# Optimization experiments

Hardware: AMD Instinct MI355X
Metric: run time of the kernel (lower is better)

## Reference

```python
import jax, jax.numpy as jnp
import numpy as np

TOPK = 10
NC = 80
ALPHA = 1.0
BETA = 6.0
EPS = 1e-8
IOU_EPS = 1e-7


def setup_inputs() -> dict:
    key = jax.random.key(0)
    ks = jax.random.split(key, 7)
    B, M, C = 32, 40, NC
    img = 640
    pts = []
    for s in (8, 16, 32):
        n = img // s
        xs = (jnp.arange(n, dtype=jnp.float32) + 0.5) * s
        gy, gx = jnp.meshgrid(xs, xs, indexing="ij")
        pts.append(jnp.stack([gx.ravel(), gy.ravel()], axis=-1))
    anchor_points = jnp.concatenate(pts, axis=0)  # (8400, 2)
    A = anchor_points.shape[0]
    pred_scores = jax.random.uniform(ks[0], (B, A, C), dtype=jnp.float32)
    ctr = anchor_points[None] + jax.random.normal(ks[1], (B, A, 2), dtype=jnp.float32) * 8.0
    wh = jax.random.uniform(ks[2], (B, A, 2), minval=16.0, maxval=128.0, dtype=jnp.float32)
    pred_boxes = jnp.concatenate([ctr - wh / 2, ctr + wh / 2], axis=-1)
    gctr = jax.random.uniform(ks[3], (B, M, 2), minval=64.0, maxval=576.0, dtype=jnp.float32)
    gwh = jax.random.uniform(ks[4], (B, M, 2), minval=32.0, maxval=256.0, dtype=jnp.float32)
    gt_boxes = jnp.concatenate([gctr - gwh / 2, gctr + gwh / 2], axis=-1)
    gt_labels = jax.random.randint(ks[5], (B, M, 1), 0, C)
    gt_mask = jax.random.uniform(ks[6], (B, M, 1)) < 0.8
    return {
        "pred_scores": pred_scores,
        "pred_boxes": pred_boxes,
        "anchor_points": anchor_points,
        "gt_labels": gt_labels,
        "gt_boxes": gt_boxes,
        "gt_mask": gt_mask,
    }


def reference(pred_scores, pred_boxes, anchor_points, gt_labels, gt_boxes, gt_mask):
    B, A, C = pred_scores.shape
    M = gt_boxes.shape[1]
    dt = pred_scores.dtype
    gtm = gt_mask[..., 0].astype(dt)  # (B, M)
    cls = gt_labels[..., 0].astype(jnp.int32)  # (B, M)
    b_idx = jnp.arange(B)[:, None]

    # --- step 1: anchor centers inside GT boxes ---
    lt = gt_boxes[:, :, None, :2]  # (B, M, 1, 2)
    rb = gt_boxes[:, :, None, 2:]
    ap = anchor_points[None, None, :, :]  # (1, 1, A, 2)
    deltas = jnp.concatenate([ap - lt, rb - ap], axis=-1)  # (B, M, A, 4)
    in_gt = (jnp.min(deltas, axis=-1) > EPS).astype(dt)  # (B, M, A)
    valid = in_gt * gtm[:, :, None]

    # --- alignment metric: cls score gathered per GT label, IoU(gt, pred) ---
    scores = pred_scores[b_idx, :, cls] * valid  # (B, M, A)
    gt = gt_boxes[:, :, None, :]  # (B, M, 1, 4)
    pd = pred_boxes[:, None, :, :]  # (B, 1, A, 4)
    iw = jnp.clip(jnp.minimum(gt[..., 2], pd[..., 2]) - jnp.maximum(gt[..., 0], pd[..., 0]), 0.0)
    ih = jnp.clip(jnp.minimum(gt[..., 3], pd[..., 3]) - jnp.maximum(gt[..., 1], pd[..., 1]), 0.0)
    inter = iw * ih
    area_g = (gt[..., 2] - gt[..., 0]) * (gt[..., 3] - gt[..., 1])
    area_p = (pd[..., 2] - pd[..., 0]) * (pd[..., 3] - pd[..., 1])
    ious = jnp.clip(inter / (area_g + area_p - inter + IOU_EPS), 0.0) * valid  # (B, M, A)
    align = (scores ** ALPHA) * (ious ** BETA)

    # --- step 2: top-k candidates per GT with duplicate suppression ---
    _, topk_idxs = jax.lax.top_k(align, TOPK)  # (B, M, K)
    km = jnp.broadcast_to(gt_mask[..., 0][:, :, None], topk_idxs.shape)
    topk_idxs = jnp.where(km, topk_idxs, 0)
    counts = jnp.zeros((B, M, A), dtype=jnp.int32)
    counts = counts.at[b_idx[:, :, None], jnp.arange(M)[None, :, None], topk_idxs].add(1)
    counts = jnp.where(counts > 1, 0, counts)
    mask = counts.astype(dt) * in_gt * gtm[:, :, None]  # (B, M, A)

    # --- step 4: resolve anchors assigned to multiple GTs by highest IoU ---
    fg = mask.sum(axis=1)  # (B, A)
    max_iou_onehot = jax.nn.one_hot(jnp.argmax(ious, axis=1), M, axis=1, dtype=dt)
    mask = jnp.where(fg[:, None, :] > 1, max_iou_onehot, mask)
    fg = mask.sum(axis=1)
    tgt_idx = jnp.argmax(mask, axis=1)  # (B, A)

    # --- targets ---
    target_labels = jnp.clip(jnp.take_along_axis(cls, tgt_idx, axis=1), 0, NC)  # (B, A)
    target_boxes = jnp.take_along_axis(gt_boxes, tgt_idx[..., None], axis=1)  # (B, A, 4)
    target_scores = jax.nn.one_hot(target_labels, NC, dtype=dt)
    target_scores = jnp.where(fg[..., None] > 0, target_scores, 0.0)

    # --- normalize scores by aligned metric ---
    align = align * mask
    pos_align = jnp.max(align, axis=-1, keepdims=True)  # (B, M, 1)
    pos_iou = jnp.max(ious * mask, axis=-1, keepdims=True)
    norm = jnp.max(align * pos_iou / (pos_align + EPS), axis=-2)[..., None]  # (B, A, 1)
    target_scores = target_scores * norm
    return target_labels, target_boxes, target_scores, fg > 0
```

## Files before the change

### kernel.cpp

```cpp
#include <hip/hip_runtime.h>
#include <cstdint>

#define TOPK_K 10
#define NCLS   80
#define EPS_F     1e-8f
#define IOU_EPS_F 1e-7f

typedef unsigned long long u64;

#define INS10(val, idx)                                                     \
    {                                                                       \
        u64 key = ((u64)__float_as_uint(val) << 32) |                       \
                  (unsigned)(~(unsigned)(idx));                             \
        if (key > kk[9]) {                                                  \
            _Pragma("unroll")                                               \
            for (int q = 0; q < 10; ++q) {                                  \
                if (key > kk[q]) { u64 t_ = kk[q]; kk[q] = key; key = t_; } \
            }                                                               \
        }                                                                   \
    }

__global__ void k_init(const unsigned char* __restrict__ gm, int n,
                       int* __restrict__ gmask,
                       unsigned int* __restrict__ pos_a,
                       unsigned int* __restrict__ pos_i,
                       u64* __restrict__ mask_bits, int BA)
{
    const int stride = gridDim.x * blockDim.x;
    for (int i = blockIdx.x * blockDim.x + threadIdx.x; i < BA; i += stride)
        mask_bits[i] = 0ull;

    if (blockIdx.x == 0) {
        __shared__ int anynz;
        if (threadIdx.x == 0) anynz = 0;
        __syncthreads();
        for (int i = threadIdx.x; i < n; i += blockDim.x) {
            if ((i & 3) && gm[i]) anynz = 1;
        }
        __syncthreads();
        const int is_int32 = (anynz == 0);
        const int* gi = (const int*)gm;
        for (int i = threadIdx.x; i < n; i += blockDim.x) {
            gmask[i] = is_int32 ? (gi[i] != 0) : (gm[i] != 0);
            pos_a[i] = 0u;
            pos_i[i] = 0u;
        }
    }
}

__global__ __launch_bounds__(256) void k_topk_geo(
    const float*  __restrict__ ps,
    const float4* __restrict__ pb,
    const int*    __restrict__ gl,
    const float4* __restrict__ gb,
    const int*    __restrict__ gmask,
    u64*          __restrict__ mask_bits,
    int B, int A, int C, int M)
{
    const int bm = blockIdx.x;
    if (!gmask[bm]) return;
    const int b = bm / M;
    const int m = bm - b * M;
    const int tid = threadIdx.x;

    const float4 g = gb[bm];
    const float areag = (g.z - g.x) * (g.w - g.y);
    const int cls = gl[bm];
    const float*  psb = ps + (size_t)b * A * C + cls;
    const float4* pbb = pb + (size_t)b * A;

    u64 kk[10];
#pragma unroll
    for (int q = 0; q < 10; ++q) kk[q] = 0ull;

    if (tid < 64) {
        const float x = (tid + 0.5f) * 8.0f;
        const float y = 4.0f;
        const float d = fminf(fminf(x - g.x, y - g.y),
                              fminf(g.z - x, g.w - y));
        const u64 inb  = __ballot(d > EPS_F);
        const u64 outb = ~inb;
        if (((outb >> tid) & 1ull) &&
            __popcll(outb & ((1ull << tid) - 1ull)) < TOPK_K) {
            INS10(0.0f, tid);
        }
    }

#define LEVEL(SS, NN, BASE)                                                   \
    {                                                                         \
        const float s_ = (float)(SS); const int n_ = (NN);                    \
        const int jlo = max(0,      (int)floorf(g.x / s_ - 0.5f));            \
        const int jhi = min(n_ - 1, (int)ceilf (g.z / s_ - 0.5f));            \
        const int ilo = max(0,      (int)floorf(g.y / s_ - 0.5f));            \
        const int ihi = min(n_ - 1, (int)ceilf (g.w / s_ - 0.5f));            \
        const int nx = jhi - jlo + 1, ny = ihi - ilo + 1;                     \
        const int tot = (nx > 0 && ny > 0) ? nx * ny : 0;                     \
        for (int c = tid; c < tot; c += 256) {                                \
            const int ci = c / nx, cj = c - ci * nx;                          \
            const int i = ilo + ci, j = jlo + cj;                             \
            const float x = (j + 0.5f) * s_, y = (i + 0.5f) * s_;             \
            const float d = fminf(fminf(x - g.x, y - g.y),                    \
                                  fminf(g.z - x, g.w - y));                   \
            if (d > EPS_F) {                                                  \
                const int a = (BASE) + i * n_ + j;                            \
                const float4 p = pbb[a];                                      \
                const float iw = fmaxf(fminf(g.z, p.z) - fmaxf(g.x, p.x), 0.f);\
                const float ih = fmaxf(fminf(g.w, p.w) - fmaxf(g.y, p.y), 0.f);\
                const float inter = iw * ih;                                  \
                const float areap = (p.z - p.x) * (p.w - p.y);                \
                const float iou = fmaxf(inter / (areag + areap - inter + IOU_EPS_F), 0.f); \
                const float sc = psb[(size_t)a * C];                          \
                const float i2 = iou * iou;                                   \
                const float al = sc * (i2 * i2 * i2);                         \
                INS10(al, a);                                                 \
            }                                                                 \
        }                                                                     \
    }
    LEVEL(8,  80, 0)
    LEVEL(16, 40, 6400)
    LEVEL(32, 20, 8000)
#undef LEVEL

    __shared__ u64 swv[4];
    const u64 bit = 1ull << m;
    for (int r = 0; r < TOPK_K; ++r) {
        u64 cur = kk[0];
#pragma unroll
        for (int off = 32; off; off >>= 1) {
            const u64 o = __shfl_xor(cur, off);
            cur = (o > cur) ? o : cur;
        }
        if ((tid & 63) == 0) swv[tid >> 6] = cur;
        __syncthreads();
        const u64 w01 = (swv[0] > swv[1]) ? swv[0] : swv[1];
        const u64 w23 = (swv[2] > swv[3]) ? swv[2] : swv[3];
        const u64 win = (w01 > w23) ? w01 : w23;
        if (kk[0] == win) {
#pragma unroll
            for (int q = 0; q < 9; ++q) kk[q] = kk[q + 1];
            kk[9] = 0ull;
        }
        if (tid == 0 && win != 0ull) {
            const unsigned a = ~(unsigned)(win & 0xFFFFFFFFull);
            float x, y;
            if (a < 6400u) {
                const unsigned i = a / 80u, j = a - i * 80u;
                x = (j + 0.5f) * 8.0f;  y = (i + 0.5f) * 8.0f;
            } else if (a < 8000u) {
                const unsigned rr = a - 6400u;
                const unsigned i = rr / 40u, j = rr - i * 40u;
                x = (j + 0.5f) * 16.0f; y = (i + 0.5f) * 16.0f;
            } else {
                const unsigned rr = a - 8000u;
                const unsigned i = rr / 20u, j = rr - i * 20u;
                x = (j + 0.5f) * 32.0f; y = (i + 0.5f) * 32.0f;
            }
            const float d = fminf(fminf(x - g.x, y - g.y),
                                  fminf(g.z - x, g.w - y));
            if (d > EPS_F)
                atomicOr(&mask_bits[(size_t)b * A + a], bit);
        }
        __syncthreads();
    }
}

__global__ __launch_bounds__(256) void k_topk_fb(
    const float*  __restrict__ ps, const float4* __restrict__ pb,
    const float2* __restrict__ apts, const int* __restrict__ gl,
    const float4* __restrict__ gb, const int* __restrict__ gmask,
    u64* __restrict__ mask_bits, int B, int A, int C, int M)
{
    const int bm = blockIdx.x;
    if (!gmask[bm]) return;
    const int b = bm / M;
    const int m = bm - b * M;
    const float4 g = gb[bm];
    const float areag = (g.z - g.x) * (g.w - g.y);
    const int cls = gl[bm];
    const float*  psb = ps + (size_t)b * A * C + cls;
    const float4* pbb = pb + (size_t)b * A;
    const int tid = threadIdx.x;

    u64 kk[10];
#pragma unroll
    for (int q = 0; q < 10; ++q) kk[q] = 0ull;

    for (int a = tid; a < A; a += 256) {
        const float2 an = apts[a];
        const float d = fminf(fminf(an.x - g.x, an.y - g.y),
                              fminf(g.z - an.x, g.w - an.y));
        float al = 0.0f;
        if (d > EPS_F) {
            const float4 p = pbb[a];
            const float iw = fmaxf(fminf(g.z, p.z) - fmaxf(g.x, p.x), 0.0f);
            const float ih = fmaxf(fminf(g.w, p.w) - fmaxf(g.y, p.y), 0.0f);
            const float inter = iw * ih;
            const float areap = (p.z - p.x) * (p.w - p.y);
            const float iou = fmaxf(inter / (areag + areap - inter + IOU_EPS_F), 0.0f);
            const float sc = psb[(size_t)a * C];
            const float i2 = iou * iou;
            al = sc * (i2 * i2 * i2);
        }
        INS10(al, a);
    }

    __shared__ u64 swv[4];
    const u64 bit = 1ull << m;
    for (int r = 0; r < TOPK_K; ++r) {
        u64 cur = kk[0];
#pragma unroll
        for (int off = 32; off; off >>= 1) {
            const u64 o = __shfl_xor(cur, off);
            cur = (o > cur) ? o : cur;
        }
        if ((tid & 63) == 0) swv[tid >> 6] = cur;
        __syncthreads();
        const u64 w01 = (swv[0] > swv[1]) ? swv[0] : swv[1];
        const u64 w23 = (swv[2] > swv[3]) ? swv[2] : swv[3];
        const u64 win = (w01 > w23) ? w01 : w23;
        if (kk[0] == win) {
#pragma unroll
            for (int q = 0; q < 9; ++q) kk[q] = kk[q + 1];
            kk[9] = 0ull;
        }
        if (tid == 0 && win != 0ull) {
            const unsigned a = ~(unsigned)(win & 0xFFFFFFFFull);
            const float2 an = apts[a];
            const float d = fminf(fminf(an.x - g.x, an.y - g.y),
                                  fminf(g.z - an.x, g.w - an.y));
            if (d > EPS_F)
                atomicOr(&mask_bits[(size_t)b * A + a], bit);
        }
        __syncthreads();
    }
}

__global__ __launch_bounds__(256) void k_resolve(
    const float*  __restrict__ ps,
    const float4* __restrict__ pb,
    const float2* __restrict__ apts,
    const int*    __restrict__ gl,
    const float4* __restrict__ gb,
    const int*    __restrict__ gmask,
    const u64*    __restrict__ mask_bits,
    int*          __restrict__ assign,
    float*        __restrict__ aval,
    unsigned int* __restrict__ pos_align,
    unsigned int* __restrict__ pos_iou,
    float*        __restrict__ out,
    int B, int A, int C, int M)
{
    const int id = blockIdx.x * blockDim.x + threadIdx.x;
    if (id >= B * A) return;
    const int b = id / A;
    const int a = id - b * A;

    const u64 bits = mask_bits[id];

    if (bits == 0ull) {
        assign[id] = 0;
        aval[id]   = 0.0f;
        int lab = gl[b * M];
        lab = lab < 0 ? 0 : (lab > NCLS ? NCLS : lab);
        out[id] = (float)lab;
        ((float4*)(out + (size_t)B * A))[id] = gb[b * M];
        out[(size_t)B * A * (5 + NCLS) + id] = 0.0f;
        return;
    }

    const int cnt = __popcll(bits);
    int t;
    const float2 an = apts[a];
    const float4 p  = pb[id];
    const float areap = (p.z - p.x) * (p.w - p.y);

    if (cnt == 1) {
        t = __ffsll(bits) - 1;
    } else {
        float best = -1.0f; int bi = 0;
        for (int mm = 0; mm < M; ++mm) {
            const float4 gg = gb[b * M + mm];
            const float d = fminf(fminf(an.x - gg.x, an.y - gg.y),
                                  fminf(gg.z - an.x, gg.w - an.y));
            float iou = 0.0f;
            if (d > EPS_F && gmask[b * M + mm]) {
                const float iw = fmaxf(fminf(gg.z, p.z) - fmaxf(gg.x, p.x), 0.0f);
                const float ih = fmaxf(fminf(gg.w, p.w) - fmaxf(gg.y, p.y), 0.0f);
                const float inter = iw * ih;
                const float areag = (gg.z - gg.x) * (gg.w - gg.y);
                iou = fmaxf(inter / (areag + areap - inter + IOU_EPS_F), 0.0f);
            }
            if (iou > best) { best = iou; bi = mm; }
        }
        t = bi;
    }

    float av = 0.0f;
    {
        const float4 gg = gb[b * M + t];
        const float d = fminf(fminf(an.x - gg.x, an.y - gg.y),
                              fminf(gg.z - an.x, gg.w - an.y));
        if (d > EPS_F && gmask[b * M + t]) {
            const float iw = fmaxf(fminf(gg.z, p.z) - fmaxf(gg.x, p.x), 0.0f);
            const float ih = fmaxf(fminf(gg.w, p.w) - fmaxf(gg.y, p.y), 0.0f);
            const float inter = iw * ih;
            const float areag = (gg.z - gg.x) * (gg.w - gg.y);
            const float iou = fmaxf(inter / (areag + areap - inter + IOU_EPS_F), 0.0f);
            const float sc = ps[((size_t)b * A + a) * C + gl[b * M + t]];
            const float i2 = iou * iou;
            av = sc * (i2 * i2 * i2);
            if (av  > 0.0f) atomicMax(&pos_align[b * M + t], __float_as_uint(av));
            if (iou > 0.0f) atomicMax(&pos_iou[b * M + t],  __float_as_uint(iou));
        }
    }

    assign[id] = t;
    aval[id]   = av;

    int lab = gl[b * M + t];
    lab = lab < 0 ? 0 : (lab > NCLS ? NCLS : lab);
    out[id] = (float)lab;
    ((float4*)(out + (size_t)B * A))[id] = gb[b * M + t];
    out[(size_t)B * A * (5 + NCLS) + id] = 1.0f;
}

__global__ void k_scores2(const int* __restrict__ assign,
                          const float* __restrict__ aval,
                          const unsigned int* __restrict__ pos_align,
                          const unsigned int* __restrict__ pos_iou,
                          const int* __restrict__ gl,
                          float4* __restrict__ scores,
                          int BA, int A, int M, int C4)
{
    const int gid = blockIdx.x * blockDim.x + threadIdx.x;
    if (gid >= BA * C4) return;
    const int row = gid / C4;
    const int c4  = gid - row * C4;
    const int b   = row / A;
    const int t   = assign[row];
    const float av = aval[row];
    const float pa = __uint_as_float(pos_align[b * M + t]);
    const float pi = __uint_as_float(pos_iou[b * M + t]);
    const float nv = av * pi / (pa + EPS_F);
    int lab = gl[b * M + t];
    lab = lab < 0 ? 0 : (lab > NCLS ? NCLS : lab);
    const int cb = c4 * 4;
    float4 v;
    v.x = (cb + 0 == lab) ? nv : 0.0f;
    v.y = (cb + 1 == lab) ? nv : 0.0f;
    v.z = (cb + 2 == lab) ? nv : 0.0f;
    v.w = (cb + 3 == lab) ? nv : 0.0f;
    scores[gid] = v;
}

extern "C" void kernel_launch(void* const* d_in, const int* in_sizes, int n_in,
                              void* d_out, int out_size, void* d_ws, size_t ws_size,
                              hipStream_t stream)
{
    const float*  ps = (const float*)d_in[0];
    const float4* pb = (const float4*)d_in[1];
    const float2* ap = (const float2*)d_in[2];
    const int*    gl = (const int*)d_in[3];
    const float4* gb = (const float4*)d_in[4];
    const unsigned char* gm = (const unsigned char*)d_in[5];

    const int A = in_sizes[2] / 2;
    const int B = in_sizes[1] / (A * 4);
    const int M = in_sizes[4] / (B * 4);
    const int C = in_sizes[0] / (B * A);
    const int BA = B * A;
    const int C4 = C / 4;

    size_t off = 0;
    auto alloc = [&](size_t bytes) {
        void* p = (char*)d_ws + off;
        off += (bytes + 255) & ~(size_t)255;
        return p;
    };
    u64*   mask_bits = (u64*)alloc((size_t)BA * 8);
    unsigned int* pos_a = (unsigned int*)alloc((size_t)B * M * 4);
    unsigned int* pos_i = (unsigned int*)alloc((size_t)B * M * 4);
    int*   gmask  = (int*)alloc((size_t)B * M * 4);
    int*   assign = (int*)alloc((size_t)BA * 4);
    float* aval   = (float*)alloc((size_t)BA * 4);
    (void)off;

    float* out = (float*)d_out;

    k_init<<<128, 256, 0, stream>>>(gm, B * M, gmask, pos_a, pos_i,
                                    mask_bits, BA);

    if (A == 8400 && C == NCLS && M <= 64) {
        k_topk_geo<<<B * M, 256, 0, stream>>>(ps, pb, gl, gb, gmask,
                                              mask_bits, B, A, C, M);
    } else {
        k_topk_fb<<<B * M, 256, 0, stream>>>(ps, pb, ap, gl, gb, gmask,
                                             mask_bits, B, A, C, M);
    }

    k_resolve<<<(BA + 255) / 256, 256, 0, stream>>>(
        ps, pb, ap, gl, gb, gmask, mask_bits,
        assign, aval, pos_a, pos_i, out, B, A, C, M);

    const int tot = BA * C4;
    k_scores2<<<(tot + 255) / 256, 256, 0, stream>>>(
        assign, aval, pos_a, pos_i, gl,
        (float4*)(out + (size_t)BA * 5), BA, A, M, C4);
}
```

Measured before the change: 205.9 us.

## Replace per-anchor bitmask atomics with per-GT winner lists and wave-per-GT top-k

Top-k selection now uses one 64-lane wave per GT instead of a 256-thread block, which removes the shared-memory cross-wave merge and the block barriers in each of the ten selection rounds. Winners are written to a compact per-GT list rather than atomically OR-ed into a per-anchor 64-bit mask, so zeroing the large B*A mask buffer is no longer needed. The resolve kernel rebuilds each anchor's bitmask by scanning the per-batch winner list held in shared memory, and it caches GT boxes, labels and masks there too. The score writes use nontemporal stores. In exchange, each resolve thread does an M*10 compare scan, and a single wave must cover the anchors of large boxes on its own.

```diff
diff --git a/kernel.cpp b/kernel.cpp
--- a/kernel.cpp
+++ b/kernel.cpp
@@ -7,6 +7,7 @@
 #define IOU_EPS_F 1e-7f
 
 typedef unsigned long long u64;
+typedef float nfloat4 __attribute__((ext_vector_type(4)));
 
 #define INS10(val, idx)                                                     \
     {                                                                       \
@@ -23,28 +24,21 @@
 __global__ void k_init(const unsigned char* __restrict__ gm, int n,
                        int* __restrict__ gmask,
                        unsigned int* __restrict__ pos_a,
-                       unsigned int* __restrict__ pos_i,
-                       u64* __restrict__ mask_bits, int BA)
-{
-    const int stride = gridDim.x * blockDim.x;
-    for (int i = blockIdx.x * blockDim.x + threadIdx.x; i < BA; i += stride)
-        mask_bits[i] = 0ull;
-
-    if (blockIdx.x == 0) {
-        __shared__ int anynz;
-        if (threadIdx.x == 0) anynz = 0;
-        __syncthreads();
-        for (int i = threadIdx.x; i < n; i += blockDim.x) {
-            if ((i & 3) && gm[i]) anynz = 1;
-        }
-        __syncthreads();
-        const int is_int32 = (anynz == 0);
-        const int* gi = (const int*)gm;
-        for (int i = threadIdx.x; i < n; i += blockDim.x) {
-            gmask[i] = is_int32 ? (gi[i] != 0) : (gm[i] != 0);
-            pos_a[i] = 0u;
-            pos_i[i] = 0u;
-        }
+                       unsigned int* __restrict__ pos_i)
+{
+    __shared__ int anynz;
+    if (threadIdx.x == 0) anynz = 0;
+    __syncthreads();
+    for (int i = threadIdx.x; i < n; i += blockDim.x) {
+        if ((i & 3) && gm[i]) anynz = 1;
+    }
+    __syncthreads();
+    const int is_int32 = (anynz == 0);
+    const int* gi = (const int*)gm;
+    for (int i = threadIdx.x; i < n; i += blockDim.x) {
+        gmask[i] = is_int32 ? (gi[i] != 0) : (gm[i] != 0);
+        pos_a[i] = 0u;
+        pos_i[i] = 0u;
     }
 }
 
@@ -54,14 +48,18 @@
     const int*    __restrict__ gl,
     const float4* __restrict__ gb,
     const int*    __restrict__ gmask,
-    u64*          __restrict__ mask_bits,
+    int*          __restrict__ wl,
     int B, int A, int C, int M)
 {
-    const int bm = blockIdx.x;
-    if (!gmask[bm]) return;
+    const int wid  = (blockIdx.x * blockDim.x + threadIdx.x) >> 6;
+    const int lane = threadIdx.x & 63;
+    if (wid >= B * M) return;
+    const int bm = wid;
+    if (!gmask[bm]) {
+        if (lane < TOPK_K) wl[bm * TOPK_K + lane] = -1;
+        return;
+    }
     const int b = bm / M;
-    const int m = bm - b * M;
-    const int tid = threadIdx.x;
 
     const float4 g = gb[bm];
     const float areag = (g.z - g.x) * (g.w - g.y);
@@ -73,16 +71,15 @@
 #pragma unroll
     for (int q = 0; q < 10; ++q) kk[q] = 0ull;
 
-    if (tid < 64) {
-        const float x = (tid + 0.5f) * 8.0f;
+    {
+        const float x = (lane + 0.5f) * 8.0f;
         const float y = 4.0f;
         const float d = fminf(fminf(x - g.x, y - g.y),
                               fminf(g.z - x, g.w - y));
-        const u64 inb  = __ballot(d > EPS_F);
-        const u64 outb = ~inb;
-        if (((outb >> tid) & 1ull) &&
-            __popcll(outb & ((1ull << tid) - 1ull)) < TOPK_K) {
-            INS10(0.0f, tid);
+        const u64 outb = ~__ballot(d > EPS_F);
+        if (((outb >> lane) & 1ull) &&
+            __popcll(outb & ((1ull << lane) - 1ull)) < TOPK_K) {
+            INS10(0.0f, lane);
         }
     }
 
@@ -95,7 +92,7 @@
         const int ihi = min(n_ - 1, (int)ceilf (g.w / s_ - 0.5f));            \
         const int nx = jhi - jlo + 1, ny = ihi - ilo + 1;                     \
         const int tot = (nx > 0 && ny > 0) ? nx * ny : 0;                     \
-        for (int c = tid; c < tot; c += 256) {                                \
+        for (int c = lane; c < tot; c += 64) {                                \
             const int ci = c / nx, cj = c - ci * nx;                          \
             const int i = ilo + ci, j = jlo + cj;                             \
             const float x = (j + 0.5f) * s_, y = (i + 0.5f) * s_;             \
@@ -121,8 +118,6 @@
     LEVEL(32, 20, 8000)
 #undef LEVEL
 
-    __shared__ u64 swv[4];
-    const u64 bit = 1ull << m;
     for (int r = 0; r < TOPK_K; ++r) {
         u64 cur = kk[0];
 #pragma unroll
@@ -130,37 +125,34 @@
             const u64 o = __shfl_xor(cur, off);
             cur = (o > cur) ? o : cur;
         }
-        if ((tid & 63) == 0) swv[tid >> 6] = cur;
-        __syncthreads();
-        const u64 w01 = (swv[0] > swv[1]) ? swv[0] : swv[1];
-        const u64 w23 = (swv[2] > swv[3]) ? swv[2] : swv[3];
-        const u64 win = (w01 > w23) ? w01 : w23;
-        if (kk[0] == win) {
+        if (kk[0] == cur) {
 #pragma unroll
             for (int q = 0; q < 9; ++q) kk[q] = kk[q + 1];
             kk[9] = 0ull;
         }
-        if (tid == 0 && win != 0ull) {
-            const unsigned a = ~(unsigned)(win & 0xFFFFFFFFull);
-            float x, y;
-            if (a < 6400u) {
-                const unsigned i = a / 80u, j = a - i * 80u;
-                x = (j + 0.5f) * 8.0f;  y = (i + 0.5f) * 8.0f;
-            } else if (a < 8000u) {
-                const unsigned rr = a - 6400u;
-                const unsigned i = rr / 40u, j = rr - i * 40u;
-                x = (j + 0.5f) * 16.0f; y = (i + 0.5f) * 16.0f;
-            } else {
-                const unsigned rr = a - 8000u;
-                const unsigned i = rr / 20u, j = rr - i * 20u;
-                x = (j + 0.5f) * 32.0f; y = (i + 0.5f) * 32.0f;
+        if (lane == 0) {
+            int wa = -1;
+            if (cur != 0ull) {
+                const unsigned a = ~(unsigned)(cur & 0xFFFFFFFFull);
+                float x, y;
+                if (a < 6400u) {
+                    const unsigned i = a / 80u, j = a - i * 80u;
+                    x = (j + 0.5f) * 8.0f;  y = (i + 0.5f) * 8.0f;
+                } else if (a < 8000u) {
+                    const unsigned rr = a - 6400u;
+                    const unsigned i = rr / 40u, j = rr - i * 40u;
+                    x = (j + 0.5f) * 16.0f; y = (i + 0.5f) * 16.0f;
+                } else {
+                    const unsigned rr = a - 8000u;
+                    const unsigned i = rr / 20u, j = rr - i * 20u;
+                    x = (j + 0.5f) * 32.0f; y = (i + 0.5f) * 32.0f;
+                }
+                const float d = fminf(fminf(x - g.x, y - g.y),
+                                      fminf(g.z - x, g.w - y));
+                if (d > EPS_F) wa = (int)a;
             }
-            const float d = fminf(fminf(x - g.x, y - g.y),
-                                  fminf(g.z - x, g.w - y));
-            if (d > EPS_F)
-                atomicOr(&mask_bits[(size_t)b * A + a], bit);
-        }
-        __syncthreads();
+            wl[bm * TOPK_K + r] = wa;
+        }
     }
 }
 
@@ -168,24 +160,28 @@
     const float*  __restrict__ ps, const float4* __restrict__ pb,
     const float2* __restrict__ apts, const int* __restrict__ gl,
     const float4* __restrict__ gb, const int* __restrict__ gmask,
-    u64* __restrict__ mask_bits, int B, int A, int C, int M)
-{
-    const int bm = blockIdx.x;
-    if (!gmask[bm]) return;
+    int* __restrict__ wl, int B, int A, int C, int M)
+{
+    const int wid  = (blockIdx.x * blockDim.x + threadIdx.x) >> 6;
+    const int lane = threadIdx.x & 63;
+    if (wid >= B * M) return;
+    const int bm = wid;
+    if (!gmask[bm]) {
+        if (lane < TOPK_K) wl[bm * TOPK_K + lane] = -1;
+        return;
+    }
     const int b = bm / M;
-    const int m = bm - b * M;
     const float4 g = gb[bm];
     const float areag = (g.z - g.x) * (g.w - g.y);
     const int cls = gl[bm];
     const float*  psb = ps + (size_t)b * A * C + cls;
     const float4* pbb = pb + (size_t)b * A;
-    const int tid = threadIdx.x;
 
     u64 kk[10];
 #pragma unroll
     for (int q = 0; q < 10; ++q) kk[q] = 0ull;
 
-    for (int a = tid; a < A; a += 256) {
+    for (int a = lane; a < A; a += 64) {
         const float2 an = apts[a];
         const float d = fminf(fminf(an.x - g.x, an.y - g.y),
                               fminf(g.z - an.x, g.w - an.y));
@@ -204,8 +200,6 @@
         INS10(al, a);
     }
 
-    __shared__ u64 swv[4];
-    const u64 bit = 1ull << m;
     for (int r = 0; r < TOPK_K; ++r) {
         u64 cur = kk[0];
 #pragma unroll
@@ -213,25 +207,22 @@
             const u64 o = __shfl_xor(cur, off);
             cur = (o > cur) ? o : cur;
         }
-        if ((tid & 63) == 0) swv[tid >> 6] = cur;
-        __syncthreads();
-        const u64 w01 = (swv[0] > swv[1]) ? swv[0] : swv[1];
-        const u64 w23 = (swv[2] > swv[3]) ? swv[2] : swv[3];
-        const u64 win = (w01 > w23) ? w01 : w23;
-        if (kk[0] == win) {
+        if (kk[0] == cur) {
 #pragma unroll
             for (int q = 0; q < 9; ++q) kk[q] = kk[q + 1];
             kk[9] = 0ull;
         }
-        if (tid == 0 && win != 0ull) {
-            const unsigned a = ~(unsigned)(win & 0xFFFFFFFFull);
-            const float2 an = apts[a];
-            const float d = fminf(fminf(an.x - g.x, an.y - g.y),
-                                  fminf(g.z - an.x, g.w - an.y));
-            if (d > EPS_F)
-                atomicOr(&mask_bits[(size_t)b * A + a], bit);
-        }
-        __syncthreads();
+        if (lane == 0) {
+            int wa = -1;
+            if (cur != 0ull) {
+                const unsigned a = ~(unsigned)(cur & 0xFFFFFFFFull);
+                const float2 an = apts[a];
+                const float d = fminf(fminf(an.x - g.x, an.y - g.y),
+                                      fminf(g.z - an.x, g.w - an.y));
+                if (d > EPS_F) wa = (int)a;
+            }
+            wl[bm * TOPK_K + r] = wa;
+        }
     }
 }
 
@@ -242,28 +233,49 @@
     const int*    __restrict__ gl,
     const float4* __restrict__ gb,
     const int*    __restrict__ gmask,
-    const u64*    __restrict__ mask_bits,
+    const int*    __restrict__ wl,
     int*          __restrict__ assign,
     float*        __restrict__ aval,
     unsigned int* __restrict__ pos_align,
     unsigned int* __restrict__ pos_iou,
     float*        __restrict__ out,
-    int B, int A, int C, int M)
-{
-    const int id = blockIdx.x * blockDim.x + threadIdx.x;
-    if (id >= B * A) return;
-    const int b = id / A;
-    const int a = id - b * A;
-
-    const u64 bits = mask_bits[id];
+    int B, int A, int C, int M, int NCHK)
+{
+    const int b    = blockIdx.x / NCHK;
+    const int chnk = blockIdx.x - b * NCHK;
+    const int tid  = threadIdx.x;
+    const int a    = chnk * 256 + tid;
+
+    __shared__ int    swl[64 * TOPK_K];
+    __shared__ float4 sgb[64];
+    __shared__ int    sgl[64];
+    __shared__ int    sgm[64];
+
+    for (int i = tid; i < M * TOPK_K; i += 256) swl[i] = wl[b * M * TOPK_K + i];
+    if (tid < M) {
+        sgb[tid] = gb[b * M + tid];
+        sgl[tid] = gl[b * M + tid];
+        sgm[tid] = gmask[b * M + tid];
+    }
+    __syncthreads();
+    if (a >= A) return;
+    const int id = b * A + a;
+
+    u64 bits = 0ull;
+    for (int m = 0; m < M; ++m) {
+        int hit = 0;
+#pragma unroll
+        for (int k = 0; k < TOPK_K; ++k) hit |= (swl[m * TOPK_K + k] == a);
+        bits |= (u64)(hit != 0) << m;
+    }
 
     if (bits == 0ull) {
         assign[id] = 0;
         aval[id]   = 0.0f;
-        int lab = gl[b * M];
+        int lab = sgl[0];
         lab = lab < 0 ? 0 : (lab > NCLS ? NCLS : lab);
         out[id] = (float)lab;
-        ((float4*)(out + (size_t)B * A))[id] = gb[b * M];
+        ((float4*)(out + (size_t)B * A))[id] = sgb[0];
         out[(size_t)B * A * (5 + NCLS) + id] = 0.0f;
         return;
     }
@@ -279,11 +291,11 @@
     } else {
         float best = -1.0f; int bi = 0;
         for (int mm = 0; mm < M; ++mm) {
-            const float4 gg = gb[b * M + mm];
+            const float4 gg = sgb[mm];
             const float d = fminf(fminf(an.x - gg.x, an.y - gg.y),
                                   fminf(gg.z - an.x, gg.w - an.y));
             float iou = 0.0f;
-            if (d > EPS_F && gmask[b * M + mm]) {
+            if (d > EPS_F && sgm[mm]) {
                 const float iw = fmaxf(fminf(gg.z, p.z) - fmaxf(gg.x, p.x), 0.0f);
                 const float ih = fmaxf(fminf(gg.w, p.w) - fmaxf(gg.y, p.y), 0.0f);
                 const float inter = iw * ih;
@@ -297,16 +309,16 @@
 
     float av = 0.0f;
     {
-        const float4 gg = gb[b * M + t];
+        const float4 gg = sgb[t];
         const float d = fminf(fminf(an.x - gg.x, an.y - gg.y),
                               fminf(gg.z - an.x, gg.w - an.y));
-        if (d > EPS_F && gmask[b * M + t]) {
+        if (d > EPS_F && sgm[t]) {
             const float iw = fmaxf(fminf(gg.z, p.z) - fmaxf(gg.x, p.x), 0.0f);
             const float ih = fmaxf(fminf(gg.w, p.w) - fmaxf(gg.y, p.y), 0.0f);
             const float inter = iw * ih;
             const float areag = (gg.z - gg.x) * (gg.w - gg.y);
             const float iou = fmaxf(inter / (areag + areap - inter + IOU_EPS_F), 0.0f);
-            const float sc = ps[((size_t)b * A + a) * C + gl[b * M + t]];
+            const float sc = ps[((size_t)b * A + a) * C + sgl[t]];
             const float i2 = iou * iou;
             av = sc * (i2 * i2 * i2);
             if (av  > 0.0f) atomicMax(&pos_align[b * M + t], __float_as_uint(av));
@@ -317,10 +329,10 @@
     assign[id] = t;
     aval[id]   = av;
 
-    int lab = gl[b * M + t];
+    int lab = sgl[t];
     lab = lab < 0 ? 0 : (lab > NCLS ? NCLS : lab);
     out[id] = (float)lab;
-    ((float4*)(out + (size_t)B * A))[id] = gb[b * M + t];
+    ((float4*)(out + (size_t)B * A))[id] = sgb[t];
     out[(size_t)B * A * (5 + NCLS) + id] = 1.0f;
 }
 
@@ -329,7 +341,7 @@
                           const unsigned int* __restrict__ pos_align,
                           const unsigned int* __restrict__ pos_iou,
                           const int* __restrict__ gl,
-                          float4* __restrict__ scores,
+                          float* __restrict__ scores,
                           int BA, int A, int M, int C4)
 {
     const int gid = blockIdx.x * blockDim.x + threadIdx.x;
@@ -345,12 +357,12 @@
     int lab = gl[b * M + t];
     lab = lab < 0 ? 0 : (lab > NCLS ? NCLS : lab);
     const int cb = c4 * 4;
-    float4 v;
+    nfloat4 v;
     v.x = (cb + 0 == lab) ? nv : 0.0f;
     v.y = (cb + 1 == lab) ? nv : 0.0f;
     v.z = (cb + 2 == lab) ? nv : 0.0f;
     v.w = (cb + 3 == lab) ? nv : 0.0f;
-    scores[gid] = v;
+    __builtin_nontemporal_store(v, (nfloat4*)(scores + (size_t)gid * 4));
 }
 
 extern "C" void kernel_launch(void* const* d_in, const int* in_sizes, int n_in,
@@ -377,33 +389,34 @@
         off += (bytes + 255) & ~(size_t)255;
         return p;
     };
-    u64*   mask_bits = (u64*)alloc((size_t)BA * 8);
     unsigned int* pos_a = (unsigned int*)alloc((size_t)B * M * 4);
     unsigned int* pos_i = (unsigned int*)alloc((size_t)B * M * 4);
     int*   gmask  = (int*)alloc((size_t)B * M * 4);
+    int*   wl     = (int*)alloc((size_t)B * M * TOPK_K * 4);
     int*   assign = (int*)alloc((size_t)BA * 4);
     float* aval   = (float*)alloc((size_t)BA * 4);
     (void)off;
 
     float* out = (float*)d_out;
 
-    k_init<<<128, 256, 0, stream>>>(gm, B * M, gmask, pos_a, pos_i,
-                                    mask_bits, BA);
-
+    k_init<<<1, 256, 0, stream>>>(gm, B * M, gmask, pos_a, pos_i);
+
+    const int topk_blocks = (B * M * 64 + 255) / 256;
     if (A == 8400 && C == NCLS && M <= 64) {
-        k_topk_geo<<<B * M, 256, 0, stream>>>(ps, pb, gl, gb, gmask,
-                                              mask_bits, B, A, C, M);
+        k_topk_geo<<<topk_blocks, 256, 0, stream>>>(ps, pb, gl, gb, gmask,
+                                                    wl, B, A, C, M);
     } else {
-        k_topk_fb<<<B * M, 256, 0, stream>>>(ps, pb, ap, gl, gb, gmask,
-                                             mask_bits, B, A, C, M);
-    }
-
-    k_resolve<<<(BA + 255) / 256, 256, 0, stream>>>(
-        ps, pb, ap, gl, gb, gmask, mask_bits,
-        assign, aval, pos_a, pos_i, out, B, A, C, M);
+        k_topk_fb<<<topk_blocks, 256, 0, stream>>>(ps, pb, ap, gl, gb, gmask,
+                                                   wl, B, A, C, M);
+    }
+
+    const int NCHK = (A + 255) / 256;
+    k_resolve<<<B * NCHK, 256, 0, stream>>>(
+        ps, pb, ap, gl, gb, gmask, wl,
+        assign, aval, pos_a, pos_i, out, B, A, C, M, NCHK);
 
     const int tot = BA * C4;
     k_scores2<<<(tot + 255) / 256, 256, 0, stream>>>(
         assign, aval, pos_a, pos_i, gl,
-        (float4*)(out + (size_t)BA * 5), BA, A, M, C4);
-}
+        out + (size_t)BA * 5, BA, A, M, C4);
+}
```

Measured after the change: 212.5 us. 3.2% more time.
